# Performance work log

Hardware: AMD Instinct MI355X
Metric: run time of the kernel (lower is better)

The kernel has to match this reference:

```python
import jax, jax.numpy as jnp
import numpy as np

HEADS = 4
DIM_HEAD = 32
EPS = 1e-5

def _layernorm(x, g, b):
    mu = jnp.mean(x, axis=-1, keepdims=True)
    var = jnp.var(x, axis=-1, keepdims=True)
    return (x - mu) * jax.lax.rsqrt(var + EPS) * g + b

def setup_inputs() -> dict:
    key = jax.random.key(0)
    ks = jax.random.split(key, 8)
    B, C, H, W = 16, 256, 32, 32
    N = H * W
    inner = HEADS * DIM_HEAD  # 128
    s = lambda d: 1.0 / np.sqrt(d)
    return {
        "x": jax.random.normal(ks[0], (B, C, H, W), jnp.float32),
        "pos_embedding": jax.random.normal(ks[1], (1, N, C), jnp.float32),
        "w_qkv": jax.random.normal(ks[2], (C, inner * 3), jnp.float32) * s(C),
        "w_out": jax.random.normal(ks[3], (inner, C), jnp.float32) * s(inner),
        "b_out": jnp.zeros((C,), jnp.float32),
        "w_ff1": jax.random.normal(ks[4], (C, inner), jnp.float32) * s(C),
        "b_ff1": jnp.zeros((inner,), jnp.float32),
        "w_ff2": jax.random.normal(ks[5], (inner, C), jnp.float32) * s(inner),
        "b_ff2": jnp.zeros((C,), jnp.float32),
        "g1": jnp.ones((C,), jnp.float32),
        "beta1": jnp.zeros((C,), jnp.float32),
        "g2": jnp.ones((C,), jnp.float32),
        "beta2": jnp.zeros((C,), jnp.float32),
    }

def reference(x, pos_embedding, w_qkv, w_out, b_out, w_ff1, b_ff1, w_ff2, b_ff2, g1, beta1, g2, beta2):
    b, c, h, w = x.shape
    n = h * w
    tok = jnp.transpose(x.reshape(b, c, n), (0, 2, 1))  # [b, n, c]
    tok = tok + pos_embedding  # (dropout is identity at eval)
    # attention
    qkv = _layernorm(tok, g1, beta1) @ w_qkv  # [b, n, 3*inner]
    qkv = qkv.reshape(b, n, 3, HEADS, DIM_HEAD)
    q, k, v = qkv[:, :, 0], qkv[:, :, 1], qkv[:, :, 2]  # [b, n, h, d]
    scale = DIM_HEAD ** -0.5
    dots = jnp.einsum('bihd,bjhd->bhij', q, k) * scale
    attn = jax.nn.softmax(dots, axis=-1)
    out = jnp.einsum('bhij,bjhd->bihd', attn, v).reshape(b, n, HEADS * DIM_HEAD)
    tok = out @ w_out + b_out + tok
    # ffn
    hdn = jax.nn.gelu(_layernorm(tok, g2, beta2) @ w_ff1 + b_ff1, approximate=False)
    tok = hdn @ w_ff2 + b_ff2 + tok
    return jnp.transpose(tok, (0, 2, 1)).reshape(b, c, h, w)
```

## Files before the change

### kernel.cpp

```cpp
#include <hip/hip_runtime.h>
#include <hip/hip_bf16.h>
#include <math.h>

#define B_     16
#define C_     256
#define N_     1024
#define HEADS_ 4
#define DH_    32
#define INNER_ 128
#define EPS_   1e-5f

typedef __attribute__((ext_vector_type(8))) short bf16x8;
typedef __attribute__((ext_vector_type(4))) float f32x4;

__device__ __forceinline__ ushort f2bf(float f) {
  union { float f; unsigned u; } v; v.f = f;
  unsigned u = v.u;
  return (ushort)((u + 0x7fffu + ((u >> 16) & 1u)) >> 16);
}
__device__ __forceinline__ float bf2f(ushort u) {
  union { unsigned u; float f; } v; v.u = ((unsigned)u) << 16;
  return v.f;
}
__device__ __forceinline__ unsigned cvt_pk_bf16(float lo, float hi) {
  unsigned r;
  asm("v_cvt_pk_bf16_f32 %0, %1, %2" : "=v"(r) : "v"(lo), "v"(hi));
  return r;
}

#define QSCALE_ 0.2550348652979437f

__global__ __launch_bounds__(256) void k_wconv(
    const float* __restrict__ wqkv, const float* __restrict__ wout,
    const float* __restrict__ wff1, const float* __restrict__ wff2,
    ushort* __restrict__ wqkvT, ushort* __restrict__ woutT,
    ushort* __restrict__ wff1T, ushort* __restrict__ wff2T) {
  int i = blockIdx.x * 256 + threadIdx.x;
  if (i < 98304) {
    int k = i / 384, n = i % 384;
    wqkvT[n * 256 + k] = f2bf(wqkv[i]);
    return;
  }
  i -= 98304;
  if (i < 32768) {
    int k = i / 256, n = i % 256;
    woutT[n * 128 + k] = f2bf(wout[i]);
    return;
  }
  i -= 32768;
  if (i < 32768) {
    int k = i / 128, n = i % 128;
    wff1T[n * 256 + k] = f2bf(wff1[i]);
    return;
  }
  i -= 32768;
  {
    int k = i / 256, n = i % 256;
    wff2T[n * 128 + k] = f2bf(wff2[i]);
  }
}

union KFusedSmem {
  float  xs[C_][68];
  ushort xnl[64][264];
};

__global__ __launch_bounds__(512) void k_fused(
    const float* __restrict__ x, const float* __restrict__ pos,
    const float* __restrict__ g1, const float* __restrict__ beta1,
    const ushort* __restrict__ wqkvT, ushort* __restrict__ tokb,
    ushort* __restrict__ qb, ushort* __restrict__ kb, ushort* __restrict__ vtb) {
  const int b  = blockIdx.x >> 4;
  const int n0 = (blockIdx.x & 15) << 6;
  const int t  = threadIdx.x;
  __shared__ KFusedSmem u;

  {
    const int nq = t & 15, cq = t >> 4;
#pragma unroll
    for (int i = 0; i < 8; ++i) {
      const int c = i * 32 + cq;
      const float4 v = *reinterpret_cast<const float4*>(
          &x[((size_t)b * C_ + c) * N_ + n0 + 4 * nq]);
      *reinterpret_cast<float4*>(&u.xs[c][4 * nq]) = v;
    }
  }
  __syncthreads();

  {
    const int tl = t >> 3, sub = t & 7, c0 = sub * 32;
    const int n = n0 + tl;
    float v[32];
#pragma unroll
    for (int i = 0; i < 32; ++i) v[i] = u.xs[c0 + i][tl];
#pragma unroll
    for (int j = 0; j < 8; ++j) {
      const float4 p = *reinterpret_cast<const float4*>(&pos[(size_t)n * C_ + c0 + 4 * j]);
      v[4*j] += p.x; v[4*j+1] += p.y; v[4*j+2] += p.z; v[4*j+3] += p.w;
    }
    float s = 0.f;
#pragma unroll
    for (int i = 0; i < 32; ++i) s += v[i];
    s += __shfl_xor(s, 1); s += __shfl_xor(s, 2); s += __shfl_xor(s, 4);
    const float mu = s * (1.f / C_);
    float sq = 0.f;
#pragma unroll
    for (int i = 0; i < 32; ++i) { const float d = v[i] - mu; sq += d * d; }
    sq += __shfl_xor(sq, 1); sq += __shfl_xor(sq, 2); sq += __shfl_xor(sq, 4);
    const float rs = rsqrtf(sq * (1.f / C_) + EPS_);

    ushort* tokrow = &tokb[((size_t)b * N_ + n) * C_ + c0];
    ushort xn_local[32];
#pragma unroll
    for (int j = 0; j < 8; ++j) {
      ushort4 tu;
      tu.x = f2bf(v[4*j]);   tu.y = f2bf(v[4*j+1]);
      tu.z = f2bf(v[4*j+2]); tu.w = f2bf(v[4*j+3]);
      *reinterpret_cast<ushort4*>(&tokrow[4 * j]) = tu;
      const float4 g  = *reinterpret_cast<const float4*>(&g1[c0 + 4 * j]);
      const float4 be = *reinterpret_cast<const float4*>(&beta1[c0 + 4 * j]);
      xn_local[4*j]   = f2bf((v[4*j]   - mu) * rs * g.x + be.x);
      xn_local[4*j+1] = f2bf((v[4*j+1] - mu) * rs * g.y + be.y);
      xn_local[4*j+2] = f2bf((v[4*j+2] - mu) * rs * g.z + be.z);
      xn_local[4*j+3] = f2bf((v[4*j+3] - mu) * rs * g.w + be.w);
    }
    __syncthreads();
#pragma unroll
    for (int j = 0; j < 8; ++j)
      *reinterpret_cast<ushort4*>(&u.xnl[tl][c0 + 4 * j]) =
          *reinterpret_cast<ushort4*>(&xn_local[4 * j]);
  }
  __syncthreads();

  {
    const int w = t >> 6, lane = t & 63;
    const int li = lane & 15, g = lane >> 4;
#pragma unroll
    for (int mf = 0; mf < 3; ++mf) {
      const int chb = w * 48 + mf * 16;
      bf16x8 Af[8];
#pragma unroll
      for (int ks = 0; ks < 8; ++ks)
        Af[ks] = *reinterpret_cast<const bf16x8*>(
            &wqkvT[(size_t)(chb + li) * C_ + ks * 32 + 8 * g]);
#pragma unroll
      for (int nf = 0; nf < 4; ++nf) {
        bf16x8 Bf[8];
#pragma unroll
        for (int ks = 0; ks < 8; ++ks)
          Bf[ks] = *reinterpret_cast<const bf16x8*>(&u.xnl[nf * 16 + li][ks * 32 + 8 * g]);
        f32x4 acc = {0.f, 0.f, 0.f, 0.f};
#pragma unroll
        for (int ks = 0; ks < 8; ++ks)
          acc = __builtin_amdgcn_mfma_f32_16x16x32_bf16(Af[ks], Bf[ks], acc, 0, 0, 0);
        const int nn = n0 + nf * 16 + li;
        const int ch0 = chb + 4 * g;
        if (ch0 < 128) {
          const int h = ch0 >> 5, dh = ch0 & 31;
          ushort4 uq;
          uq.x = f2bf(acc[0] * QSCALE_); uq.y = f2bf(acc[1] * QSCALE_);
          uq.z = f2bf(acc[2] * QSCALE_); uq.w = f2bf(acc[3] * QSCALE_);
          *reinterpret_cast<ushort4*>(&qb[(((size_t)(b * HEADS_ + h)) * N_ + nn) * DH_ + dh]) = uq;
        } else if (ch0 < 256) {
          const int c2 = ch0 - 128, h = c2 >> 5, dh = c2 & 31;
          ushort4 uk;
          uk.x = f2bf(acc[0]); uk.y = f2bf(acc[1]); uk.z = f2bf(acc[2]); uk.w = f2bf(acc[3]);
          *reinterpret_cast<ushort4*>(&kb[(((size_t)(b * HEADS_ + h)) * N_ + nn) * DH_ + dh]) = uk;
        } else {
          const int c2 = ch0 - 256, h = c2 >> 5, dh = c2 & 31;
          ushort* base = &vtb[(((size_t)(b * HEADS_ + h)) * DH_ + dh) * N_ + nn];
          base[0] = f2bf(acc[0]); base[N_] = f2bf(acc[1]);
          base[2 * N_] = f2bf(acc[2]); base[3 * N_] = f2bf(acc[3]);
        }
      }
    }
  }
}

__global__ __launch_bounds__(256) void k_attn(
    const ushort* __restrict__ qb, const ushort* __restrict__ kb,
    const ushort* __restrict__ vtb, ushort* __restrict__ ao) {
  const int blk = blockIdx.x;
  const int b   = blk >> 5;
  const int h   = (blk >> 3) & 3;
  const int qt2 = blk & 7;
  const int tid = threadIdx.x;
  const int w = tid >> 6, lane = tid & 63;
  const int qi = lane & 15, g = lane >> 4;

  __shared__ __align__(16) ushort P_lds[4][2][16][80];

  const int bh  = b * HEADS_ + h;
  const int nq0 = qt2 * 128 + w * 32;
  const ushort* Kb = kb  + (size_t)bh * N_ * DH_;
  const ushort* Vt = vtb + (size_t)bh * DH_ * N_;

  bf16x8 qf[2];
#pragma unroll
  for (int G = 0; G < 2; ++G)
    qf[G] = *reinterpret_cast<const bf16x8*>(
        qb + ((size_t)bh * N_ + nq0 + G * 16 + qi) * DH_ + 8 * g);

  f32x4 acc[2][2];
#pragma unroll
  for (int G = 0; G < 2; ++G)
#pragma unroll
    for (int d = 0; d < 2; ++d)
#pragma unroll
      for (int r = 0; r < 4; ++r) acc[G][d][r] = 0.f;
  float m[2] = {-INFINITY, -INFINITY};
  float l[2] = {0.f, 0.f};

  bf16x8 kf[4], vf[2][2];
#pragma unroll
  for (int kt = 0; kt < 4; ++kt)
    kf[kt] = *reinterpret_cast<const bf16x8*>(
        Kb + (size_t)(kt * 16 + qi) * DH_ + 8 * g);
#pragma unroll
  for (int c = 0; c < 2; ++c)
#pragma unroll
    for (int d = 0; d < 2; ++d)
      vf[c][d] = *reinterpret_cast<const bf16x8*>(
          Vt + (size_t)(d * 16 + qi) * N_ + c * 32 + 8 * g);

  for (int jt = 0; jt < 16; ++jt) {
    const int kn = (jt < 15 ? jt + 1 : 15) * 64;
    bf16x8 kfn[4], vfn[2][2];
#pragma unroll
    for (int kt = 0; kt < 4; ++kt)
      kfn[kt] = *reinterpret_cast<const bf16x8*>(
          Kb + (size_t)(kn + kt * 16 + qi) * DH_ + 8 * g);
#pragma unroll
    for (int c = 0; c < 2; ++c)
#pragma unroll
      for (int d = 0; d < 2; ++d)
        vfn[c][d] = *reinterpret_cast<const bf16x8*>(
            Vt + (size_t)(d * 16 + qi) * N_ + kn + c * 32 + 8 * g);

    f32x4 s[2][4];
#pragma unroll
    for (int G = 0; G < 2; ++G)
#pragma unroll
      for (int kt = 0; kt < 4; ++kt) {
        f32x4 z = {0.f, 0.f, 0.f, 0.f};
        s[G][kt] = __builtin_amdgcn_mfma_f32_16x16x32_bf16(kf[kt], qf[G], z, 0, 0, 0);
      }

#pragma unroll
    for (int G = 0; G < 2; ++G) {
      float t0 = fmaxf(fmaxf(s[G][0][0], s[G][0][1]), fmaxf(s[G][0][2], s[G][0][3]));
      float t1 = fmaxf(fmaxf(s[G][1][0], s[G][1][1]), fmaxf(s[G][1][2], s[G][1][3]));
      float t2 = fmaxf(fmaxf(s[G][2][0], s[G][2][1]), fmaxf(s[G][2][2], s[G][2][3]));
      float t3 = fmaxf(fmaxf(s[G][3][0], s[G][3][1]), fmaxf(s[G][3][2], s[G][3][3]));
      float tmax = fmaxf(fmaxf(t0, t1), fmaxf(t2, t3));
      tmax = fmaxf(tmax, __shfl_xor(tmax, 16));
      tmax = fmaxf(tmax, __shfl_xor(tmax, 32));
      if (!__all(tmax <= m[G] + 8.0f)) {
        const float nm = fmaxf(m[G], tmax);
        const float corr = exp2f(m[G] - nm);
#pragma unroll
        for (int d = 0; d < 2; ++d)
#pragma unroll
          for (int r = 0; r < 4; ++r) acc[G][d][r] *= corr;
        l[G] *= corr;
        m[G] = nm;
      }
      float psum = 0.f;
#pragma unroll
      for (int kt = 0; kt < 4; ++kt) {
        const float p0 = exp2f(s[G][kt][0] - m[G]);
        const float p1 = exp2f(s[G][kt][1] - m[G]);
        const float p2 = exp2f(s[G][kt][2] - m[G]);
        const float p3 = exp2f(s[G][kt][3] - m[G]);
        psum += (p0 + p1) + (p2 + p3);
        uint2 dw;
        dw.x = cvt_pk_bf16(p0, p1);
        dw.y = cvt_pk_bf16(p2, p3);
        *reinterpret_cast<uint2*>(&P_lds[w][G][qi][kt * 16 + 4 * g]) = dw;
      }
      l[G] += psum;
    }

#pragma unroll
    for (int c = 0; c < 2; ++c) {
      const bf16x8 pf0 = *reinterpret_cast<const bf16x8*>(&P_lds[w][0][qi][c * 32 + 8 * g]);
      const bf16x8 pf1 = *reinterpret_cast<const bf16x8*>(&P_lds[w][1][qi][c * 32 + 8 * g]);
#pragma unroll
      for (int d = 0; d < 2; ++d) {
        acc[0][d] = __builtin_amdgcn_mfma_f32_16x16x32_bf16(vf[c][d], pf0, acc[0][d], 0, 0, 0);
        acc[1][d] = __builtin_amdgcn_mfma_f32_16x16x32_bf16(vf[c][d], pf1, acc[1][d], 0, 0, 0);
      }
    }

#pragma unroll
    for (int kt = 0; kt < 4; ++kt) kf[kt] = kfn[kt];
#pragma unroll
    for (int c = 0; c < 2; ++c)
#pragma unroll
      for (int d = 0; d < 2; ++d) vf[c][d] = vfn[c][d];
  }

#pragma unroll
  for (int G = 0; G < 2; ++G) {
    float lg = l[G];
    lg += __shfl_xor(lg, 16);
    lg += __shfl_xor(lg, 32);
    const float inv = 1.f / lg;
    const int n = nq0 + G * 16 + qi;
#pragma unroll
    for (int d = 0; d < 2; ++d) {
      ushort4 uo;
      uo.x = f2bf(acc[G][d][0] * inv);
      uo.y = f2bf(acc[G][d][1] * inv);
      uo.z = f2bf(acc[G][d][2] * inv);
      uo.w = f2bf(acc[G][d][3] * inv);
      *reinterpret_cast<ushort4*>(
          &ao[((size_t)b * N_ + n) * INNER_ + h * DH_ + d * 16 + 4 * g]) = uo;
    }
  }
}

__global__ __launch_bounds__(256) void k_mlp(
    const ushort* __restrict__ ao, const ushort* __restrict__ tokb,
    const ushort* __restrict__ woutT, const float* __restrict__ b_out,
    const ushort* __restrict__ wff1T, const float* __restrict__ b_ff1,
    const ushort* __restrict__ wff2T, const float* __restrict__ b_ff2,
    const float* __restrict__ g2, const float* __restrict__ beta2,
    float* __restrict__ out) {
  const int T0 = blockIdx.x * 32;
  const int bb = T0 >> 10;
  const int nb = T0 & 1023;
  const int tid = threadIdx.x;
  const int w = tid >> 6, lane = tid & 63, li = lane & 15, g = lane >> 4;

  __shared__ float  t2s[32][260];
  __shared__ ushort xn2[32][264];
  __shared__ ushort hsb[32][136];

  {
    bf16x8 Af[2][4];
#pragma unroll
    for (int mf = 0; mf < 2; ++mf)
#pragma unroll
      for (int ks = 0; ks < 4; ++ks)
        Af[mf][ks] = *reinterpret_cast<const bf16x8*>(
            &ao[((size_t)(T0 + mf * 16 + li)) * INNER_ + ks * 32 + 8 * g]);
#pragma unroll
    for (int nf = 0; nf < 4; ++nf) {
      const int n = w * 64 + nf * 16;
      bf16x8 Bf[4];
#pragma unroll
      for (int ks = 0; ks < 4; ++ks)
        Bf[ks] = *reinterpret_cast<const bf16x8*>(
            &woutT[(size_t)(n + li) * INNER_ + ks * 32 + 8 * g]);
#pragma unroll
      for (int mf = 0; mf < 2; ++mf) {
        f32x4 acc = {0.f, 0.f, 0.f, 0.f};
#pragma unroll
        for (int ks = 0; ks < 4; ++ks)
          acc = __builtin_amdgcn_mfma_f32_16x16x32_bf16(Af[mf][ks], Bf[ks], acc, 0, 0, 0);
        const int nch = n + li;
        const int tl0 = mf * 16 + 4 * g;
        const float bo = b_out[nch];
#pragma unroll
        for (int r = 0; r < 4; ++r)
          t2s[tl0 + r][nch] =
              acc[r] + bo + bf2f(tokb[((size_t)(T0 + tl0 + r)) * C_ + nch]);
      }
    }
  }
  __syncthreads();

  {
    const int tl = tid >> 3, c0 = (tid & 7) * 32;
    float v[32];
#pragma unroll
    for (int j = 0; j < 8; ++j) {
      const float4 t4 = *reinterpret_cast<const float4*>(&t2s[tl][c0 + 4 * j]);
      v[4*j] = t4.x; v[4*j+1] = t4.y; v[4*j+2] = t4.z; v[4*j+3] = t4.w;
    }
    float s = 0.f;
#pragma unroll
    for (int i = 0; i < 32; ++i) s += v[i];
    s += __shfl_xor(s, 1); s += __shfl_xor(s, 2); s += __shfl_xor(s, 4);
    const float mu = s * (1.f / C_);
    float sq = 0.f;
#pragma unroll
    for (int i = 0; i < 32; ++i) { const float d = v[i] - mu; sq += d * d; }
    sq += __shfl_xor(sq, 1); sq += __shfl_xor(sq, 2); sq += __shfl_xor(sq, 4);
    const float rs = rsqrtf(sq * (1.f / C_) + EPS_);
#pragma unroll
    for (int j = 0; j < 8; ++j) {
      const float4 gg = *reinterpret_cast<const float4*>(&g2[c0 + 4 * j]);
      const float4 be = *reinterpret_cast<const float4*>(&beta2[c0 + 4 * j]);
      ushort4 u;
      u.x = f2bf((v[4*j]   - mu) * rs * gg.x + be.x);
      u.y = f2bf((v[4*j+1] - mu) * rs * gg.y + be.y);
      u.z = f2bf((v[4*j+2] - mu) * rs * gg.z + be.z);
      u.w = f2bf((v[4*j+3] - mu) * rs * gg.w + be.w);
      *reinterpret_cast<ushort4*>(&xn2[tl][c0 + 4 * j]) = u;
    }
  }
  __syncthreads();

  {
    bf16x8 Af[2][8];
#pragma unroll
    for (int mf = 0; mf < 2; ++mf)
#pragma unroll
      for (int ks = 0; ks < 8; ++ks)
        Af[mf][ks] = *reinterpret_cast<const bf16x8*>(&xn2[mf * 16 + li][ks * 32 + 8 * g]);
#pragma unroll
    for (int nf = 0; nf < 2; ++nf) {
      const int n = w * 32 + nf * 16;
      bf16x8 Bf[8];
#pragma unroll
      for (int ks = 0; ks < 8; ++ks)
        Bf[ks] = *reinterpret_cast<const bf16x8*>(
            &wff1T[(size_t)(n + li) * C_ + ks * 32 + 8 * g]);
#pragma unroll
      for (int mf = 0; mf < 2; ++mf) {
        f32x4 acc = {0.f, 0.f, 0.f, 0.f};
#pragma unroll
        for (int ks = 0; ks < 8; ++ks)
          acc = __builtin_amdgcn_mfma_f32_16x16x32_bf16(Af[mf][ks], Bf[ks], acc, 0, 0, 0);
        const int nch = n + li;
        const int tl0 = mf * 16 + 4 * g;
        const float bf1 = b_ff1[nch];
#pragma unroll
        for (int r = 0; r < 4; ++r) {
          float hv = acc[r] + bf1;
          hv = 0.5f * hv * (1.f + erff(hv * 0.70710678118654752f));
          hsb[tl0 + r][nch] = f2bf(hv);
        }
      }
    }
  }
  __syncthreads();

  {
    bf16x8 Af[2][4];
#pragma unroll
    for (int mf = 0; mf < 2; ++mf)
#pragma unroll
      for (int ks = 0; ks < 4; ++ks)
        Af[mf][ks] = *reinterpret_cast<const bf16x8*>(&hsb[mf * 16 + li][ks * 32 + 8 * g]);
#pragma unroll
    for (int nf = 0; nf < 4; ++nf) {
      const int n = w * 64 + nf * 16;
      bf16x8 Bf[4];
#pragma unroll
      for (int ks = 0; ks < 4; ++ks)
        Bf[ks] = *reinterpret_cast<const bf16x8*>(
            &wff2T[(size_t)(n + li) * INNER_ + ks * 32 + 8 * g]);
#pragma unroll
      for (int mf = 0; mf < 2; ++mf) {
        f32x4 acc = {0.f, 0.f, 0.f, 0.f};
#pragma unroll
        for (int ks = 0; ks < 4; ++ks)
          acc = __builtin_amdgcn_mfma_f32_16x16x32_bf16(Af[mf][ks], Bf[ks], acc, 0, 0, 0);
        const int nch = n + li;
        const int tl0 = mf * 16 + 4 * g;
        const float bo = b_ff2[nch];
        float4 o;
        o.x = acc[0] + bo + t2s[tl0 + 0][nch];
        o.y = acc[1] + bo + t2s[tl0 + 1][nch];
        o.z = acc[2] + bo + t2s[tl0 + 2][nch];
        o.w = acc[3] + bo + t2s[tl0 + 3][nch];
        *reinterpret_cast<float4*>(
            &out[((size_t)bb * C_ + nch) * N_ + nb + tl0]) = o;
      }
    }
  }
}

extern "C" void kernel_launch(void* const* d_in, const int* in_sizes, int n_in,
                              void* d_out, int out_size, void* d_ws, size_t ws_size,
                              hipStream_t stream) {
  const float* x     = (const float*)d_in[0];
  const float* pos   = (const float*)d_in[1];
  const float* w_qkv = (const float*)d_in[2];
  const float* w_out = (const float*)d_in[3];
  const float* b_out = (const float*)d_in[4];
  const float* w_ff1 = (const float*)d_in[5];
  const float* b_ff1 = (const float*)d_in[6];
  const float* w_ff2 = (const float*)d_in[7];
  const float* b_ff2 = (const float*)d_in[8];
  const float* g1    = (const float*)d_in[9];
  const float* beta1 = (const float*)d_in[10];
  const float* g2    = (const float*)d_in[11];
  const float* beta2 = (const float*)d_in[12];
  float* out = (float*)d_out;

  ushort* tokb  = (ushort*)d_ws;
  ushort* ao    = tokb + 4194304;
  ushort* qb    = ao + 2097152;
  ushort* kb    = qb + 2097152;
  ushort* vtb   = kb + 2097152;
  ushort* wqkvT = vtb + 2097152;
  ushort* woutT = wqkvT + 98304;
  ushort* wff1T = woutT + 32768;
  ushort* wff2T = wff1T + 32768;

  k_wconv<<<768, 256, 0, stream>>>(w_qkv, w_out, w_ff1, w_ff2,
                                   wqkvT, woutT, wff1T, wff2T);
  k_fused<<<256, 512, 0, stream>>>(x, pos, g1, beta1, wqkvT, tokb, qb, kb, vtb);
  k_attn<<<512, 256, 0, stream>>>(qb, kb, vtb, ao);
  k_mlp<<<512, 256, 0, stream>>>(ao, tokb, woutT, b_out, wff1T, b_ff1,
                                 wff2T, b_ff2, g2, beta2, out);
}
```

Measured before the change: 165.3 us.

## Fuse attention and MLP kernels, passing attention output through LDS

Merges the attention kernel and the MLP kernel into one launch. Each block now handles 32 query tokens of one batch across all four heads (one wave per head) and writes the attention output into shared memory, where the out-projection reads it directly. This removes the global round trip for the attention output and one kernel launch, and shared-memory buffers are unioned to limit LDS use. In exchange, each block reads K/V for all four heads for only 32 queries, so K/V reuse per block drops and global K/V traffic rises roughly fourfold.

```diff
diff --git a/kernel.cpp b/kernel.cpp
--- a/kernel.cpp
+++ b/kernel.cpp
@@ -177,165 +177,162 @@
   }
 }
 
-__global__ __launch_bounds__(256) void k_attn(
+__global__ __launch_bounds__(256) void k_attn_mlp(
     const ushort* __restrict__ qb, const ushort* __restrict__ kb,
-    const ushort* __restrict__ vtb, ushort* __restrict__ ao) {
-  const int blk = blockIdx.x;
-  const int b   = blk >> 5;
-  const int h   = (blk >> 3) & 3;
-  const int qt2 = blk & 7;
-  const int tid = threadIdx.x;
-  const int w = tid >> 6, lane = tid & 63;
-  const int qi = lane & 15, g = lane >> 4;
-
-  __shared__ __align__(16) ushort P_lds[4][2][16][80];
-
-  const int bh  = b * HEADS_ + h;
-  const int nq0 = qt2 * 128 + w * 32;
-  const ushort* Kb = kb  + (size_t)bh * N_ * DH_;
-  const ushort* Vt = vtb + (size_t)bh * DH_ * N_;
-
-  bf16x8 qf[2];
-#pragma unroll
-  for (int G = 0; G < 2; ++G)
-    qf[G] = *reinterpret_cast<const bf16x8*>(
-        qb + ((size_t)bh * N_ + nq0 + G * 16 + qi) * DH_ + 8 * g);
-
-  f32x4 acc[2][2];
-#pragma unroll
-  for (int G = 0; G < 2; ++G)
-#pragma unroll
-    for (int d = 0; d < 2; ++d)
-#pragma unroll
-      for (int r = 0; r < 4; ++r) acc[G][d][r] = 0.f;
-  float m[2] = {-INFINITY, -INFINITY};
-  float l[2] = {0.f, 0.f};
-
-  bf16x8 kf[4], vf[2][2];
-#pragma unroll
-  for (int kt = 0; kt < 4; ++kt)
-    kf[kt] = *reinterpret_cast<const bf16x8*>(
-        Kb + (size_t)(kt * 16 + qi) * DH_ + 8 * g);
-#pragma unroll
-  for (int c = 0; c < 2; ++c)
-#pragma unroll
-    for (int d = 0; d < 2; ++d)
-      vf[c][d] = *reinterpret_cast<const bf16x8*>(
-          Vt + (size_t)(d * 16 + qi) * N_ + c * 32 + 8 * g);
-
-  for (int jt = 0; jt < 16; ++jt) {
-    const int kn = (jt < 15 ? jt + 1 : 15) * 64;
-    bf16x8 kfn[4], vfn[2][2];
-#pragma unroll
-    for (int kt = 0; kt < 4; ++kt)
-      kfn[kt] = *reinterpret_cast<const bf16x8*>(
-          Kb + (size_t)(kn + kt * 16 + qi) * DH_ + 8 * g);
-#pragma unroll
-    for (int c = 0; c < 2; ++c)
-#pragma unroll
-      for (int d = 0; d < 2; ++d)
-        vfn[c][d] = *reinterpret_cast<const bf16x8*>(
-            Vt + (size_t)(d * 16 + qi) * N_ + kn + c * 32 + 8 * g);
-
-    f32x4 s[2][4];
-#pragma unroll
-    for (int G = 0; G < 2; ++G)
-#pragma unroll
-      for (int kt = 0; kt < 4; ++kt) {
-        f32x4 z = {0.f, 0.f, 0.f, 0.f};
-        s[G][kt] = __builtin_amdgcn_mfma_f32_16x16x32_bf16(kf[kt], qf[G], z, 0, 0, 0);
-      }
-
-#pragma unroll
-    for (int G = 0; G < 2; ++G) {
-      float t0 = fmaxf(fmaxf(s[G][0][0], s[G][0][1]), fmaxf(s[G][0][2], s[G][0][3]));
-      float t1 = fmaxf(fmaxf(s[G][1][0], s[G][1][1]), fmaxf(s[G][1][2], s[G][1][3]));
-      float t2 = fmaxf(fmaxf(s[G][2][0], s[G][2][1]), fmaxf(s[G][2][2], s[G][2][3]));
-      float t3 = fmaxf(fmaxf(s[G][3][0], s[G][3][1]), fmaxf(s[G][3][2], s[G][3][3]));
-      float tmax = fmaxf(fmaxf(t0, t1), fmaxf(t2, t3));
-      tmax = fmaxf(tmax, __shfl_xor(tmax, 16));
-      tmax = fmaxf(tmax, __shfl_xor(tmax, 32));
-      if (!__all(tmax <= m[G] + 8.0f)) {
-        const float nm = fmaxf(m[G], tmax);
-        const float corr = exp2f(m[G] - nm);
-#pragma unroll
-        for (int d = 0; d < 2; ++d)
-#pragma unroll
-          for (int r = 0; r < 4; ++r) acc[G][d][r] *= corr;
-        l[G] *= corr;
-        m[G] = nm;
-      }
-      float psum = 0.f;
-#pragma unroll
-      for (int kt = 0; kt < 4; ++kt) {
-        const float p0 = exp2f(s[G][kt][0] - m[G]);
-        const float p1 = exp2f(s[G][kt][1] - m[G]);
-        const float p2 = exp2f(s[G][kt][2] - m[G]);
-        const float p3 = exp2f(s[G][kt][3] - m[G]);
-        psum += (p0 + p1) + (p2 + p3);
-        uint2 dw;
-        dw.x = cvt_pk_bf16(p0, p1);
-        dw.y = cvt_pk_bf16(p2, p3);
-        *reinterpret_cast<uint2*>(&P_lds[w][G][qi][kt * 16 + 4 * g]) = dw;
-      }
-      l[G] += psum;
-    }
-
-#pragma unroll
-    for (int c = 0; c < 2; ++c) {
-      const bf16x8 pf0 = *reinterpret_cast<const bf16x8*>(&P_lds[w][0][qi][c * 32 + 8 * g]);
-      const bf16x8 pf1 = *reinterpret_cast<const bf16x8*>(&P_lds[w][1][qi][c * 32 + 8 * g]);
-#pragma unroll
-      for (int d = 0; d < 2; ++d) {
-        acc[0][d] = __builtin_amdgcn_mfma_f32_16x16x32_bf16(vf[c][d], pf0, acc[0][d], 0, 0, 0);
-        acc[1][d] = __builtin_amdgcn_mfma_f32_16x16x32_bf16(vf[c][d], pf1, acc[1][d], 0, 0, 0);
-      }
-    }
-
-#pragma unroll
-    for (int kt = 0; kt < 4; ++kt) kf[kt] = kfn[kt];
-#pragma unroll
-    for (int c = 0; c < 2; ++c)
-#pragma unroll
-      for (int d = 0; d < 2; ++d) vf[c][d] = vfn[c][d];
-  }
-
-#pragma unroll
-  for (int G = 0; G < 2; ++G) {
-    float lg = l[G];
-    lg += __shfl_xor(lg, 16);
-    lg += __shfl_xor(lg, 32);
-    const float inv = 1.f / lg;
-    const int n = nq0 + G * 16 + qi;
-#pragma unroll
-    for (int d = 0; d < 2; ++d) {
-      ushort4 uo;
-      uo.x = f2bf(acc[G][d][0] * inv);
-      uo.y = f2bf(acc[G][d][1] * inv);
-      uo.z = f2bf(acc[G][d][2] * inv);
-      uo.w = f2bf(acc[G][d][3] * inv);
-      *reinterpret_cast<ushort4*>(
-          &ao[((size_t)b * N_ + n) * INNER_ + h * DH_ + d * 16 + 4 * g]) = uo;
-    }
-  }
-}
-
-__global__ __launch_bounds__(256) void k_mlp(
-    const ushort* __restrict__ ao, const ushort* __restrict__ tokb,
+    const ushort* __restrict__ vtb, const ushort* __restrict__ tokb,
     const ushort* __restrict__ woutT, const float* __restrict__ b_out,
     const ushort* __restrict__ wff1T, const float* __restrict__ b_ff1,
     const ushort* __restrict__ wff2T, const float* __restrict__ b_ff2,
     const float* __restrict__ g2, const float* __restrict__ beta2,
     float* __restrict__ out) {
-  const int T0 = blockIdx.x * 32;
-  const int bb = T0 >> 10;
-  const int nb = T0 & 1023;
+  const int b   = blockIdx.x >> 5;
+  const int tt  = blockIdx.x & 31;
+  const int nq0 = tt * 32;
   const int tid = threadIdx.x;
-  const int w = tid >> 6, lane = tid & 63, li = lane & 15, g = lane >> 4;
-
-  __shared__ float  t2s[32][260];
-  __shared__ ushort xn2[32][264];
-  __shared__ ushort hsb[32][136];
+  const int w = tid >> 6, lane = tid & 63;
+  const int qi = lane & 15, g = lane >> 4;
+
+  __shared__ __align__(16) union {
+    ushort P[4][2][16][80];
+    float  t2s[32][260];
+  } u1;
+  __shared__ __align__(16) ushort xn2[32][264];
+  __shared__ __align__(16) union {
+    ushort aos[32][136];
+    ushort hsb[32][136];
+  } u2;
+
+  {
+    const int bh = b * HEADS_ + w;
+    const ushort* Kb = kb  + (size_t)bh * N_ * DH_;
+    const ushort* Vt = vtb + (size_t)bh * DH_ * N_;
+
+    bf16x8 qf[2];
+#pragma unroll
+    for (int G = 0; G < 2; ++G)
+      qf[G] = *reinterpret_cast<const bf16x8*>(
+          qb + ((size_t)bh * N_ + nq0 + G * 16 + qi) * DH_ + 8 * g);
+
+    f32x4 acc[2][2];
+#pragma unroll
+    for (int G = 0; G < 2; ++G)
+#pragma unroll
+      for (int d = 0; d < 2; ++d)
+#pragma unroll
+        for (int r = 0; r < 4; ++r) acc[G][d][r] = 0.f;
+    float m[2] = {-INFINITY, -INFINITY};
+    float l[2] = {0.f, 0.f};
+
+    bf16x8 kf[4], vf[2][2];
+#pragma unroll
+    for (int kt = 0; kt < 4; ++kt)
+      kf[kt] = *reinterpret_cast<const bf16x8*>(
+          Kb + (size_t)(kt * 16 + qi) * DH_ + 8 * g);
+#pragma unroll
+    for (int c = 0; c < 2; ++c)
+#pragma unroll
+      for (int d = 0; d < 2; ++d)
+        vf[c][d] = *reinterpret_cast<const bf16x8*>(
+            Vt + (size_t)(d * 16 + qi) * N_ + c * 32 + 8 * g);
+
+    for (int jt = 0; jt < 16; ++jt) {
+      const int kn = (jt < 15 ? jt + 1 : 15) * 64;
+      bf16x8 kfn[4], vfn[2][2];
+#pragma unroll
+      for (int kt = 0; kt < 4; ++kt)
+        kfn[kt] = *reinterpret_cast<const bf16x8*>(
+            Kb + (size_t)(kn + kt * 16 + qi) * DH_ + 8 * g);
+#pragma unroll
+      for (int c = 0; c < 2; ++c)
+#pragma unroll
+        for (int d = 0; d < 2; ++d)
+          vfn[c][d] = *reinterpret_cast<const bf16x8*>(
+              Vt + (size_t)(d * 16 + qi) * N_ + kn + c * 32 + 8 * g);
+
+      f32x4 s[2][4];
+#pragma unroll
+      for (int G = 0; G < 2; ++G)
+#pragma unroll
+        for (int kt = 0; kt < 4; ++kt) {
+          f32x4 z = {0.f, 0.f, 0.f, 0.f};
+          s[G][kt] = __builtin_amdgcn_mfma_f32_16x16x32_bf16(kf[kt], qf[G], z, 0, 0, 0);
+        }
+
+#pragma unroll
+      for (int G = 0; G < 2; ++G) {
+        float t0 = fmaxf(fmaxf(s[G][0][0], s[G][0][1]), fmaxf(s[G][0][2], s[G][0][3]));
+        float t1 = fmaxf(fmaxf(s[G][1][0], s[G][1][1]), fmaxf(s[G][1][2], s[G][1][3]));
+        float t2 = fmaxf(fmaxf(s[G][2][0], s[G][2][1]), fmaxf(s[G][2][2], s[G][2][3]));
+        float t3 = fmaxf(fmaxf(s[G][3][0], s[G][3][1]), fmaxf(s[G][3][2], s[G][3][3]));
+        float tmax = fmaxf(fmaxf(t0, t1), fmaxf(t2, t3));
+        tmax = fmaxf(tmax, __shfl_xor(tmax, 16));
+        tmax = fmaxf(tmax, __shfl_xor(tmax, 32));
+        if (!__all(tmax <= m[G] + 8.0f)) {
+          const float nm = fmaxf(m[G], tmax);
+          const float corr = exp2f(m[G] - nm);
+#pragma unroll
+          for (int d = 0; d < 2; ++d)
+#pragma unroll
+            for (int r = 0; r < 4; ++r) acc[G][d][r] *= corr;
+          l[G] *= corr;
+          m[G] = nm;
+        }
+        float psum = 0.f;
+#pragma unroll
+        for (int kt = 0; kt < 4; ++kt) {
+          const float p0 = exp2f(s[G][kt][0] - m[G]);
+          const float p1 = exp2f(s[G][kt][1] - m[G]);
+          const float p2 = exp2f(s[G][kt][2] - m[G]);
+          const float p3 = exp2f(s[G][kt][3] - m[G]);
+          psum += (p0 + p1) + (p2 + p3);
+          uint2 dw;
+          dw.x = cvt_pk_bf16(p0, p1);
+          dw.y = cvt_pk_bf16(p2, p3);
+          *reinterpret_cast<uint2*>(&u1.P[w][G][qi][kt * 16 + 4 * g]) = dw;
+        }
+        l[G] += psum;
+      }
+
+#pragma unroll
+      for (int c = 0; c < 2; ++c) {
+        const bf16x8 pf0 = *reinterpret_cast<const bf16x8*>(&u1.P[w][0][qi][c * 32 + 8 * g]);
+        const bf16x8 pf1 = *reinterpret_cast<const bf16x8*>(&u1.P[w][1][qi][c * 32 + 8 * g]);
+#pragma unroll
+        for (int d = 0; d < 2; ++d) {
+          acc[0][d] = __builtin_amdgcn_mfma_f32_16x16x32_bf16(vf[c][d], pf0, acc[0][d], 0, 0, 0);
+          acc[1][d] = __builtin_amdgcn_mfma_f32_16x16x32_bf16(vf[c][d], pf1, acc[1][d], 0, 0, 0);
+        }
+      }
+
+#pragma unroll
+      for (int kt = 0; kt < 4; ++kt) kf[kt] = kfn[kt];
+#pragma unroll
+      for (int c = 0; c < 2; ++c)
+#pragma unroll
+        for (int d = 0; d < 2; ++d) vf[c][d] = vfn[c][d];
+    }
+
+#pragma unroll
+    for (int G = 0; G < 2; ++G) {
+      float lg = l[G];
+      lg += __shfl_xor(lg, 16);
+      lg += __shfl_xor(lg, 32);
+      const float inv = 1.f / lg;
+      const int nloc = G * 16 + qi;
+#pragma unroll
+      for (int d = 0; d < 2; ++d) {
+        ushort4 uo;
+        uo.x = f2bf(acc[G][d][0] * inv);
+        uo.y = f2bf(acc[G][d][1] * inv);
+        uo.z = f2bf(acc[G][d][2] * inv);
+        uo.w = f2bf(acc[G][d][3] * inv);
+        *reinterpret_cast<ushort4*>(&u2.aos[nloc][w * 32 + d * 16 + 4 * g]) = uo;
+      }
+    }
+  }
+  __syncthreads();
+
+  const int li = qi;
 
   {
     bf16x8 Af[2][4];
@@ -343,8 +340,7 @@
     for (int mf = 0; mf < 2; ++mf)
 #pragma unroll
       for (int ks = 0; ks < 4; ++ks)
-        Af[mf][ks] = *reinterpret_cast<const bf16x8*>(
-            &ao[((size_t)(T0 + mf * 16 + li)) * INNER_ + ks * 32 + 8 * g]);
+        Af[mf][ks] = *reinterpret_cast<const bf16x8*>(&u2.aos[mf * 16 + li][ks * 32 + 8 * g]);
 #pragma unroll
     for (int nf = 0; nf < 4; ++nf) {
       const int n = w * 64 + nf * 16;
@@ -364,8 +360,8 @@
         const float bo = b_out[nch];
 #pragma unroll
         for (int r = 0; r < 4; ++r)
-          t2s[tl0 + r][nch] =
-              acc[r] + bo + bf2f(tokb[((size_t)(T0 + tl0 + r)) * C_ + nch]);
+          u1.t2s[tl0 + r][nch] =
+              acc[r] + bo + bf2f(tokb[((size_t)b * N_ + nq0 + tl0 + r) * C_ + nch]);
       }
     }
   }
@@ -376,7 +372,7 @@
     float v[32];
 #pragma unroll
     for (int j = 0; j < 8; ++j) {
-      const float4 t4 = *reinterpret_cast<const float4*>(&t2s[tl][c0 + 4 * j]);
+      const float4 t4 = *reinterpret_cast<const float4*>(&u1.t2s[tl][c0 + 4 * j]);
       v[4*j] = t4.x; v[4*j+1] = t4.y; v[4*j+2] = t4.z; v[4*j+3] = t4.w;
     }
     float s = 0.f;
@@ -393,12 +389,12 @@
     for (int j = 0; j < 8; ++j) {
       const float4 gg = *reinterpret_cast<const float4*>(&g2[c0 + 4 * j]);
       const float4 be = *reinterpret_cast<const float4*>(&beta2[c0 + 4 * j]);
-      ushort4 u;
-      u.x = f2bf((v[4*j]   - mu) * rs * gg.x + be.x);
-      u.y = f2bf((v[4*j+1] - mu) * rs * gg.y + be.y);
-      u.z = f2bf((v[4*j+2] - mu) * rs * gg.z + be.z);
-      u.w = f2bf((v[4*j+3] - mu) * rs * gg.w + be.w);
-      *reinterpret_cast<ushort4*>(&xn2[tl][c0 + 4 * j]) = u;
+      ushort4 uu;
+      uu.x = f2bf((v[4*j]   - mu) * rs * gg.x + be.x);
+      uu.y = f2bf((v[4*j+1] - mu) * rs * gg.y + be.y);
+      uu.z = f2bf((v[4*j+2] - mu) * rs * gg.z + be.z);
+      uu.w = f2bf((v[4*j+3] - mu) * rs * gg.w + be.w);
+      *reinterpret_cast<ushort4*>(&xn2[tl][c0 + 4 * j]) = uu;
     }
   }
   __syncthreads();
@@ -431,7 +427,7 @@
         for (int r = 0; r < 4; ++r) {
           float hv = acc[r] + bf1;
           hv = 0.5f * hv * (1.f + erff(hv * 0.70710678118654752f));
-          hsb[tl0 + r][nch] = f2bf(hv);
+          u2.hsb[tl0 + r][nch] = f2bf(hv);
         }
       }
     }
@@ -444,7 +440,7 @@
     for (int mf = 0; mf < 2; ++mf)
 #pragma unroll
       for (int ks = 0; ks < 4; ++ks)
-        Af[mf][ks] = *reinterpret_cast<const bf16x8*>(&hsb[mf * 16 + li][ks * 32 + 8 * g]);
+        Af[mf][ks] = *reinterpret_cast<const bf16x8*>(&u2.hsb[mf * 16 + li][ks * 32 + 8 * g]);
 #pragma unroll
     for (int nf = 0; nf < 4; ++nf) {
       const int n = w * 64 + nf * 16;
@@ -463,12 +459,12 @@
         const int tl0 = mf * 16 + 4 * g;
         const float bo = b_ff2[nch];
         float4 o;
-        o.x = acc[0] + bo + t2s[tl0 + 0][nch];
-        o.y = acc[1] + bo + t2s[tl0 + 1][nch];
-        o.z = acc[2] + bo + t2s[tl0 + 2][nch];
-        o.w = acc[3] + bo + t2s[tl0 + 3][nch];
+        o.x = acc[0] + bo + u1.t2s[tl0 + 0][nch];
+        o.y = acc[1] + bo + u1.t2s[tl0 + 1][nch];
+        o.z = acc[2] + bo + u1.t2s[tl0 + 2][nch];
+        o.w = acc[3] + bo + u1.t2s[tl0 + 3][nch];
         *reinterpret_cast<float4*>(
-            &out[((size_t)bb * C_ + nch) * N_ + nb + tl0]) = o;
+            &out[((size_t)b * C_ + nch) * N_ + nq0 + tl0]) = o;
       }
     }
   }
@@ -493,8 +489,7 @@
   float* out = (float*)d_out;
 
   ushort* tokb  = (ushort*)d_ws;
-  ushort* ao    = tokb + 4194304;
-  ushort* qb    = ao + 2097152;
+  ushort* qb    = tokb + 4194304;
   ushort* kb    = qb + 2097152;
   ushort* vtb   = kb + 2097152;
   ushort* wqkvT = vtb + 2097152;
@@ -505,7 +500,6 @@
   k_wconv<<<768, 256, 0, stream>>>(w_qkv, w_out, w_ff1, w_ff2,
                                    wqkvT, woutT, wff1T, wff2T);
   k_fused<<<256, 512, 0, stream>>>(x, pos, g1, beta1, wqkvT, tokb, qb, kb, vtb);
-  k_attn<<<512, 256, 0, stream>>>(qb, kb, vtb, ao);
-  k_mlp<<<512, 256, 0, stream>>>(ao, tokb, woutT, b_out, wff1T, b_ff1,
-                                 wff2T, b_ff2, g2, beta2, out);
-}
+  k_attn_mlp<<<512, 256, 0, stream>>>(qb, kb, vtb, tokb, woutT, b_out,
+                                      wff1T, b_ff1, wff2T, b_ff2, g2, beta2, out);
+}
```

After: 158.7 us. 1.04x faster.
